# Performance work log

Measured on AMD Instinct MI355X. Metric: run time of the kernel, lower is better.

The kernel has to match this reference:

```python
import jax, jax.numpy as jnp
import numpy as np

B, D, N, H = 2, 512, 2048, 8
DK = D // H
EPS = 1e-5


def conv1x1(x, w, b):
    # kernel-size-1 Conv1d == channel-mixing GEMM: (o,i) x (b,i,n) -> (b,o,n)
    return jnp.einsum('oi,bin->bon', w, x) + b[None, :, None]


def setup_inputs() -> dict:
    key = jax.random.key(0)
    ks = jax.random.split(key, 20)
    s = 0.02
    return {
        'init_query': jax.random.normal(ks[0], (B, D, N), jnp.float32),
        'key_t': jax.random.normal(ks[1], (B, D, N), jnp.float32),
        'value': jax.random.normal(ks[2], (B, D, N), jnp.float32),
        'mask': jax.random.randint(ks[3], (B, 1, N, N), 0, 2, jnp.int32),
        'Wq': jax.random.normal(ks[4], (D, D), jnp.float32) * s,
        'bq': jax.random.normal(ks[5], (D,), jnp.float32) * s,
        'Wk': jax.random.normal(ks[6], (D, D), jnp.float32) * s,
        'bk': jax.random.normal(ks[7], (D,), jnp.float32) * s,
        'Wv': jax.random.normal(ks[8], (D, D), jnp.float32) * s,
        'bv': jax.random.normal(ks[9], (D,), jnp.float32) * s,
        'Wm': jax.random.normal(ks[10], (D, D), jnp.float32) * s,
        'bm': jax.random.normal(ks[11], (D,), jnp.float32) * s,
        'W1': jax.random.normal(ks[12], (2 * D, 2 * D), jnp.float32) * s,
        'b1': jax.random.normal(ks[13], (2 * D,), jnp.float32) * s,
        'gamma': jnp.ones((2 * D,), jnp.float32),
        'beta': jnp.zeros((2 * D,), jnp.float32),
        'rmean': jax.random.normal(ks[14], (2 * D,), jnp.float32) * s,
        'rvar': jnp.abs(jax.random.normal(ks[15], (2 * D,), jnp.float32)) * 0.1 + 0.5,
        'W2': jax.random.normal(ks[16], (D, 2 * D), jnp.float32) * s,
        'b2': jnp.zeros((D,), jnp.float32),  # nn.init.constant_(bias, 0.0)
    }


def reference(init_query, key_t, value, mask, Wq, bq, Wk, bk, Wv, bv, Wm, bm,
              W1, b1, gamma, beta, rmean, rvar, W2, b2):
    # projections, split channels into (d_k, n_heads) exactly like torch .view
    q = conv1x1(init_query, Wq, bq).reshape(B, DK, H, N)
    k = conv1x1(key_t, Wk, bk).reshape(B, DK, H, N)
    v = conv1x1(value, Wv, bv).reshape(B, DK, H, N)
    scores = jnp.einsum('bdhn,bdhm->bhnm', q, k) / jnp.sqrt(jnp.float32(DK))
    scores = jnp.where(mask == 0, jnp.float32(-1e9), scores)
    attn = jax.nn.softmax(scores, axis=-1)
    x = jnp.einsum('bhnm,bdhm->bdhn', attn, v).reshape(B, D, N)
    x = conv1x1(x, Wm, bm)
    x = jnp.concatenate([x, init_query], axis=1)  # (B, 2D, N)
    h = conv1x1(x, W1, b1)
    # BatchNorm1d (inference mode with running stats) + ReLU
    h = (h - rmean[None, :, None]) * (gamma / jnp.sqrt(rvar + EPS))[None, :, None] + beta[None, :, None]
    h = jax.nn.relu(h)
    return conv1x1(h, W2, b2)
```

## Files before the change

### kernel.cpp

```cpp
#include <hip/hip_runtime.h>

typedef unsigned short u16;
typedef unsigned int u32;
typedef unsigned long long u64;
typedef long long i64;
typedef __bf16 bf16x8 __attribute__((ext_vector_type(8)));
typedef u16 u16x8 __attribute__((ext_vector_type(8)));
typedef float f32x4 __attribute__((ext_vector_type(4)));
typedef float f32x16 __attribute__((ext_vector_type(16)));

#define DEV __device__ __forceinline__

constexpr int BB = 2, DD = 512, NN = 2048, HH = 8, DKc = 64, D2 = 1024;

constexpr float QSC = 0.125f * 1.44269504088896340736f;

constexpr i64 MB = 1048576;
constexpr i64 OFF_CAT = 0;
constexpr i64 OFF_XKT = 8 * MB;
constexpr i64 OFF_XVT = 12 * MB;
constexpr i64 OFF_QH  = 16 * MB;
constexpr i64 OFF_KH  = 20 * MB;
constexpr i64 OFF_VT  = 24 * MB;
constexpr i64 OFF_HT  = 28 * MB;
constexpr i64 OFF_OP  = 36 * MB;
constexpr i64 OFF_LP  = 68 * MB;
constexpr i64 OFF_WQP = 69 * MB;
constexpr i64 OFF_WKP = 69 * MB + 524288;
constexpr i64 OFF_WVP = 69 * MB + 1048576;
constexpr i64 OFF_WMT = 69 * MB + 1572864;
constexpr i64 OFF_W1A = 71 * MB;
constexpr i64 OFF_W1C = 72 * MB;
constexpr i64 OFF_W2B = 74 * MB;
constexpr i64 OFF_BQP = 75 * MB;
constexpr i64 OFF_BKP = 75 * MB + 2048;
constexpr i64 OFF_BVP = 75 * MB + 4096;
constexpr i64 OFF_BNA = 75 * MB + 8192;
constexpr i64 OFF_BNC = 75 * MB + 12288;
constexpr i64 OFF_MSK = 76 * MB;

DEV u16 f2bf(float f) {
  u32 u = __float_as_uint(f);
  u = u + 0x7FFFu + ((u >> 16) & 1u);
  return (u16)(u >> 16);
}

DEV float bf2f(u16 u) { return __uint_as_float(((u32)u) << 16); }

DEV u32 packbf(float lo, float hi) {
  return __builtin_amdgcn_perm(__float_as_uint(hi), __float_as_uint(lo), 0x07060302u);
}

DEV float fexp2(float x) {
#if __has_builtin(__builtin_amdgcn_exp2f)
  return __builtin_amdgcn_exp2f(x);
#else
  return exp2f(x);
#endif
}

DEV bf16x8 ldfrag(const u16* p) {
  bf16x8 v;
  __builtin_memcpy(&v, __builtin_assume_aligned(p, 16), 16);
  return v;
}

DEV bf16x8 ldfrag8(const u16* p) {
  bf16x8 v;
  __builtin_memcpy(&v, __builtin_assume_aligned(p, 8), 16);
  return v;
}

DEV bf16x8 ones8() {
  u16x8 u = {0x3F80, 0x3F80, 0x3F80, 0x3F80, 0x3F80, 0x3F80, 0x3F80, 0x3F80};
  bf16x8 v;
  __builtin_memcpy(&v, &u, 16);
  return v;
}

DEV void gload16(const void* g, void* lds) {
  __builtin_amdgcn_global_load_lds((__attribute__((address_space(1))) void*)g,
                                   (__attribute__((address_space(3))) void*)lds, 16, 0, 0);
}

DEV f32x4 mfma16(bf16x8 a, bf16x8 b, f32x4 c) {
  return __builtin_amdgcn_mfma_f32_16x16x32_bf16(a, b, c, 0, 0, 0);
}

DEV f32x16 mfma32(bf16x8 a, bf16x8 b, f32x16 c) {
  return __builtin_amdgcn_mfma_f32_32x32x16_bf16(a, b, c, 0, 0, 0);
}

__global__ __launch_bounds__(256) void prep_all(
    const float* __restrict__ Wq, const float* __restrict__ Wk, const float* __restrict__ Wv,
    const float* __restrict__ Wm, const float* __restrict__ W1, const float* __restrict__ W2,
    const float* __restrict__ bq, const float* __restrict__ bk, const float* __restrict__ bv,
    const float* __restrict__ bm, const float* __restrict__ b1, const float* __restrict__ gamma_,
    const float* __restrict__ beta_, const float* __restrict__ rmean,
    const float* __restrict__ rvar, const int* __restrict__ mask,
    const float* __restrict__ iq, const float* __restrict__ kt, const float* __restrict__ vv,
    u16* __restrict__ wqp, u16* __restrict__ wkp, u16* __restrict__ wvp, u16* __restrict__ wmt,
    u16* __restrict__ w1a, u16* __restrict__ w1c, u16* __restrict__ w2b,
    float* __restrict__ bqp, float* __restrict__ bkp, float* __restrict__ bvp,
    float* __restrict__ bna, float* __restrict__ bnc, u32* __restrict__ mw,
    u16* __restrict__ cat, u16* __restrict__ xkt, u16* __restrict__ xvt) {
  __shared__ float tile[32][33];
  const int blk = blockIdx.x, t = threadIdx.x;
  if (blk < 768) {
    const int which = blk >> 8, lb = blk & 255;
    const float* W = which == 0 ? Wq : (which == 1 ? Wk : Wv);
    u16* dst = which == 0 ? wqp : (which == 1 ? wkp : wvp);
    for (int e = lb * 256 + t; e < 262144; e += 65536) {
      int op = e >> 9, i = e & 511;
      int dk = op & 63, h = op >> 6;
      dst[e] = f2bf(W[(dk * 8 + h) * 512 + i]);
    }
  } else if (blk < 1024) {
    const int lb = blk - 768;
    for (int e = lb * 256 + t; e < 262144; e += 65536) {
      int cp = e >> 9, o = e & 511;
      int dk = cp & 63, h = cp >> 6;
      wmt[e] = f2bf(Wm[o * 512 + dk * 8 + h]);
    }
  } else if (blk < 1280) {
    const int lb = blk - 1024;
    for (int e = lb * 256 + t; e < 524288; e += 65536) {
      int row = e >> 9, o = e & 511;
      w1a[e] = f2bf(W1[(i64)row * 1024 + o]);
    }
  } else if (blk < 1536) {
    const int lb = blk - 1280;
    for (int e = lb * 256 + t; e < 524288; e += 65536) {
      int row = e >> 9, j = e & 511;
      w1c[(i64)row * 1024 + 512 + j] = f2bf(W1[(i64)row * 1024 + 512 + j]);
    }
  } else if (blk < 1792) {
    const int lb = blk - 1536;
    for (int e = lb * 256 + t; e < 524288; e += 65536) w2b[e] = f2bf(W2[e]);
  } else if (blk < 1808) {
    __shared__ float sm[4][64];
    const int base = (blk - 1792) * 64;
    const int el = t & 63, oq = t >> 6;
    const float* wrow = W1 + (i64)(base + el) * 1024 + oq * 128;
    const float* bmq = bm + oq * 128;
    float s = 0.f;
#pragma unroll 8
    for (int j = 0; j < 128; j += 4) {
      float4 x = *(const float4*)(wrow + j);
      float4 y = *(const float4*)(bmq + j);
      s += x.x * y.x + x.y * y.y + x.z * y.z + x.w * y.w;
    }
    sm[oq][el] = s;
    __syncthreads();
    if (t < 64) {
      int e = base + t;
      float a = gamma_[e] * rsqrtf(rvar[e] + 1e-5f);
      bna[e] = a;
      bnc[e] = (b1[e] - rmean[e]) * a + beta_[e] + a * (sm[0][t] + sm[1][t] + sm[2][t] + sm[3][t]);
    }
  } else if (blk == 1808) {
    for (int e = t; e < 512; e += 256) {
      int src = (e & 63) * 8 + (e >> 6);
      bqp[e] = bq[src]; bkp[e] = bk[src]; bvp[e] = bv[src];
    }
  } else if (blk < 2833) {
    const int tid = (blk - 1809) * 256 + t;
    const int l = tid & 63, mt = (tid >> 6) & 31, g = (tid >> 11) & 63, b = tid >> 17;
    const int kv0 = mt * 64 + (l & 31);
    u32 word = 0;
#pragma unroll
    for (int reg = 0; reg < 16; ++reg) {
      int r = (reg & 3) + 8 * (reg >> 2) + 4 * (l >> 5);
      const int* mp = mask + ((i64)b * NN + g * 32 + r) * NN + kv0;
      word |= (mp[0] != 0 ? (1u << (2 * reg)) : 0u) | (mp[32] != 0 ? (2u << (2 * reg)) : 0u);
    }
    mw[tid] = word;
  } else {
    const int idx = blk - 2833;
    const int bx = idx & 63, by = (idx >> 6) & 15, bz = idx >> 10;
    const int tensor = bz >> 1, b = bz & 1;
    const float* src = (tensor == 0 ? iq : (tensor == 1 ? kt : vv)) + (i64)b * DD * NN;
    u16* dst; i64 ldd; int coff;
    if (tensor == 0)      { dst = cat + (i64)b * NN * D2; ldd = D2; coff = DD; }
    else if (tensor == 1) { dst = xkt + (i64)b * NN * DD; ldd = DD; coff = 0; }
    else                  { dst = xvt + (i64)b * NN * DD; ldd = DD; coff = 0; }
    const int x0 = bx * 32, y0 = by * 32;
    const int col = t & 31, rg = t >> 5;
#pragma unroll
    for (int i = 0; i < 4; ++i) {
      int row = rg + i * 8;
      tile[row][col] = src[(i64)(y0 + row) * NN + x0 + col];
    }
    __syncthreads();
    const int dp = t & 15, rbase = t >> 4;
    u32* dst32 = (u32*)dst;
    const i64 ldw = ldd >> 1;
    const int cw = (coff + y0) >> 1;
#pragma unroll
    for (int i = 0; i < 2; ++i) {
      int rr = rbase + i * 16;
      dst32[(i64)(x0 + rr) * ldw + cw + dp] = packbf(tile[2 * dp][rr], tile[2 * dp + 1][rr]);
    }
  }
}

template <int AM, int AN>
DEV void gemm_core(const u16* __restrict__ A, i64 lda, const u16* __restrict__ Bp, i64 ldb,
                   int K, u16* As, u16* Bs, f32x4 (&acc)[AM][AN]) {
  constexpr int BM = AM * 32, BN = AN * 32;
  const int t = threadIdx.x, w = t >> 6, l = t & 63, quad = l >> 4, l15 = l & 15;
  const int wm = (w >> 1) * AM * 16, wn = (w & 1) * AN * 16;
  for (int kk = 0; kk < K; kk += 64) {
    __syncthreads();
#pragma unroll
    for (int j = 0; j < BM / 32; ++j) {
      int ch = j * 256 + w * 64 + l, r = ch >> 3, c = ch & 7;
      gload16(A + (i64)r * lda + kk + ((c ^ (r & 7)) << 3), As + (j * 256 + w * 64) * 8);
    }
#pragma unroll
    for (int j = 0; j < BN / 32; ++j) {
      int ch = j * 256 + w * 64 + l, r = ch >> 3, c = ch & 7;
      gload16(Bp + (i64)r * ldb + kk + ((c ^ (r & 7)) << 3), Bs + (j * 256 + w * 64) * 8);
    }
    __syncthreads();
#pragma unroll
    for (int kc = 0; kc < 2; ++kc) {
      const int sw = ((kc * 4 + quad) ^ (l15 & 7)) << 3;
      bf16x8 af[AM], bfr[AN];
#pragma unroll
      for (int i = 0; i < AM; ++i) af[i] = ldfrag(&As[(wm + i * 16 + l15) * 64 + sw]);
#pragma unroll
      for (int j = 0; j < AN; ++j) bfr[j] = ldfrag(&Bs[(wn + j * 16 + l15) * 64 + sw]);
#pragma unroll
      for (int i = 0; i < AM; ++i)
#pragma unroll
        for (int j = 0; j < AN; ++j) acc[i][j] = mfma16(af[i], bfr[j], acc[i][j]);
    }
  }
}

__global__ __launch_bounds__(256) void qkv_gemm(const u16* __restrict__ cat,
                                                const u16* __restrict__ xkt,
                                                const u16* __restrict__ xvt,
                                                const u16* __restrict__ wqp,
                                                const u16* __restrict__ wkp,
                                                const u16* __restrict__ wvp,
                                                const u16* __restrict__ w1a,
                                                const u16* __restrict__ wmt,
                                                const float* __restrict__ bqp,
                                                const float* __restrict__ bkp,
                                                const float* __restrict__ bvp,
                                                u16* __restrict__ qh, u16* __restrict__ kh,
                                                u16* __restrict__ vt, u16* __restrict__ w1c) {
  __shared__ __align__(16) u16 As[128 * 64];
  __shared__ __align__(16) u16 Bs[64 * 64];
  const int z = blockIdx.z, b = z & 1;
  const int op = (z == 6) ? 3 : (z >> 1);
  const int t = threadIdx.x, w = t >> 6, l = t & 63, quad = l >> 4, l15 = l & 15;
  const int wm = (w >> 1) * 64, wn = (w & 1) * 32;
  int mx, ny;
  const u16 *A, *Bp;
  i64 lda, ldb;
  if (op < 2) {
    mx = blockIdx.x; ny = blockIdx.y;
    A = (op == 0 ? cat + DD : xkt);
    lda = (op == 0 ? D2 : DD);
    A += (i64)b * NN * lda + (i64)mx * 128 * lda;
    Bp = (op == 0 ? wqp : wkp) + (i64)ny * 64 * DD;
    ldb = DD;
  } else if (op == 2) {
    int f = blockIdx.x * 8 + blockIdx.y;
    mx = f >> 5; ny = f & 31;
    A = wvp + (i64)mx * 128 * DD; lda = DD;
    Bp = xvt + (i64)b * NN * DD + (i64)ny * 64 * DD; ldb = DD;
  } else {
    if (blockIdx.x >= 8) return;
    mx = blockIdx.x; ny = blockIdx.y;
    A = w1a + (i64)mx * 128 * DD; lda = DD;
    Bp = wmt + (i64)ny * 64 * DD; ldb = DD;
  }
  f32x4 acc[4][2] = {};
  gemm_core<4, 2>(A, lda, Bp, ldb, DD, As, Bs, acc);

  const int rowBase = mx * 128 + wm + quad * 4;
  const int colBase = ny * 64 + wn + l15;
  if (op < 2) {
    const float* bias = (op == 0 ? bqp : bkp);
    const float sc = (op == 0 ? QSC : 1.f);
    u16* dst = (op == 0 ? qh : kh) + (i64)b * HH * NN * DKc;
#pragma unroll
    for (int j = 0; j < 2; ++j) {
      const int col = colBase + j * 16;
      const float cA = bias[col];
#pragma unroll
      for (int i = 0; i < 4; ++i)
#pragma unroll
        for (int r = 0; r < 4; ++r) {
          const int row = rowBase + i * 16 + r;
          dst[(i64)(col >> 6) * (NN * 64) + (i64)row * 64 + (col & 63)] =
              f2bf((acc[i][j][r] + cA) * sc);
        }
    }
  } else if (op == 2) {
    u16* dst = vt + (i64)b * HH * DKc * NN;
#pragma unroll
    for (int j = 0; j < 2; ++j) {
      const int col = colBase + j * 16;
      const int colp = (col & ~63) | (((col & 31) << 1) | ((col >> 5) & 1));
#pragma unroll
      for (int i = 0; i < 4; ++i)
#pragma unroll
        for (int r = 0; r < 4; ++r) {
          const int row = rowBase + i * 16 + r;
          dst[(i64)row * NN + colp] = f2bf(acc[i][j][r] + bvp[row]);
        }
    }
  } else {
#pragma unroll
    for (int j = 0; j < 2; ++j) {
      const int col = colBase + j * 16;
#pragma unroll
      for (int i = 0; i < 4; ++i)
#pragma unroll
        for (int r = 0; r < 4; ++r) {
          const int row = rowBase + i * 16 + r;
          w1c[(i64)row * D2 + col] = f2bf(acc[i][j][r]);
        }
    }
  }
}

struct GArgs {
  const u16* A; i64 lda, sAb;
  const u16* B; i64 ldb, sBb;
  void* C; i64 ldc, sCb;
  const float* p1; const float* p2;
  int K;
};

template <int MODE, int AM, int AN, int SWZ>
__global__ __launch_bounds__(256) void gemm_bt(GArgs g) {
  __shared__ __align__(16) u16 As[AM * 32 * 64];
  __shared__ __align__(16) u16 Bs[AN * 32 * 64];
  const int t = threadIdx.x, w = t >> 6, l = t & 63, quad = l >> 4, l15 = l & 15;
  const int wm = (w >> 1) * AM * 16, wn = (w & 1) * AN * 16;
  int bx = blockIdx.x, by = blockIdx.y, bz = blockIdx.z;
  if (SWZ == 1) {
    const int i = bx + (by << 3) + (bz << 8);
    const int slot = i & 7, jj = i >> 3;
    by = slot + ((jj & 3) << 3);
    const int j2 = jj >> 2;
    bx = j2 & 7;
    bz = j2 >> 3;
  }
  const u16* A = g.A + (i64)bz * g.sAb + (i64)bx * (AM * 32) * g.lda;
  const u16* Bp = g.B + (i64)bz * g.sBb + (i64)by * (AN * 32) * g.ldb;
  f32x4 acc[AM][AN] = {};
  gemm_core<AM, AN>(A, g.lda, Bp, g.ldb, g.K, As, Bs, acc);

  const int rowBase = bx * (AM * 32) + wm + quad * 4;
  const int colBase = by * (AN * 32) + wn + l15;
#pragma unroll
  for (int j = 0; j < AN; ++j) {
    const int col = colBase + j * 16;
    float cA = 0.f, cB = 0.f;
    if (MODE == 3) { cA = g.p1[col]; cB = g.p2[col]; }
#pragma unroll
    for (int i = 0; i < AM; ++i) {
#pragma unroll
      for (int r = 0; r < 4; ++r) {
        const int row = rowBase + i * 16 + r;
        float v = acc[i][j][r];
        if (MODE == 3) {
          float x = v * cA + cB;
          ((u16*)g.C + (i64)bz * g.sCb)[(i64)row * g.ldc + col] = f2bf(x > 0.f ? x : 0.f);
        } else {
          ((float*)g.C + (i64)bz * g.sCb)[(i64)row * g.ldc + col] = v + g.p1[row];
        }
      }
    }
  }
}

__global__ __launch_bounds__(256) void flash_attn(const u16* __restrict__ Qh,
                                                  const u16* __restrict__ Kh,
                                                  const u16* __restrict__ Vt,
                                                  const u32* __restrict__ MW2,
                                                  u16* __restrict__ Opart,
                                                  float* __restrict__ Lp) {
  __shared__ __align__(16) u16 Ks[64 * 64];
  __shared__ __align__(16) u16 Vs[64 * 64];
  __shared__ __align__(16) u16 Ps[4][32 * 68];
  const int t = threadIdx.x, w = t >> 6, l = t & 63, l31 = l & 31, lh = l >> 5;
  const int flat = blockIdx.x;
  const int h = flat & 7;
  const int j = flat >> 3;
  const int nt = j & 15, zz = j >> 4;
  const int b = zz >> 2, sp = zz & 3;
  const u16* Qb = Qh + ((i64)(b * HH + h) * NN + nt * 128 + w * 32) * 64;
  const u16* Kb = Kh + (i64)(b * HH + h) * NN * 64;
  const u16* Vb = Vt + (i64)(b * HH + h) * 64 * NN;
  const u32* MWb = MW2 + ((i64)(b * 64 + nt * 4 + w) * 32) * 64 + l;
  const bf16x8 ONE = ones8();
  bf16x8 qf[4];
#pragma unroll
  for (int kc = 0; kc < 4; ++kc)
    __builtin_memcpy(&qf[kc], Qb + (i64)l31 * 64 + kc * 16 + lh * 8, 16);

  f32x16 oacc0 = {}, oacc1 = {}, lacc = {};
  for (int mt = sp * 8; mt < sp * 8 + 8; ++mt) {
    __syncthreads();
#pragma unroll
    for (int j2 = 0; j2 < 2; ++j2) {
      int ch = j2 * 256 + t, r = ch >> 3, c = ch & 7;
      gload16(Kb + (i64)(mt * 64 + r) * 64 + ((c ^ (r & 7)) << 3), &Ks[ch * 8]);
      gload16(Vb + (i64)r * NN + mt * 64 + ((c ^ (r & 7)) << 3), &Vs[ch * 8]);
    }
    __syncthreads();
    f32x16 s0 = {}, s1 = {};
#pragma unroll
    for (int kc = 0; kc < 4; ++kc) {
      const int r1 = 32 + l31;
      bf16x8 k0 = ldfrag(&Ks[l31 * 64 + (((kc * 2 + lh) ^ (l31 & 7)) << 3)]);
      bf16x8 k1 = ldfrag(&Ks[r1 * 64 + (((kc * 2 + lh) ^ (r1 & 7)) << 3)]);
      s0 = mfma32(qf[kc], k0, s0);
      s1 = mfma32(qf[kc], k1, s1);
    }
    const u32 mword = MWb[(i64)mt * 64];
#pragma unroll
    for (int reg = 0; reg < 16; ++reg) {
      const int row = (reg & 3) + 8 * (reg >> 2) + 4 * lh;
      u32 sh = mword >> (2 * reg);
      u32 m01 = ((sh & 1u) | ((sh & 2u) << 15)) * 0xFFFFu;
      u32 pv = packbf(fexp2(s0[reg]), fexp2(s1[reg])) & m01;
      *(u32*)__builtin_assume_aligned(&Ps[w][row * 68 + l31 * 2], 4) = pv;
    }
    asm volatile("" ::: "memory");
    bf16x8 pf[4];
#pragma unroll
    for (int kc = 0; kc < 4; ++kc) pf[kc] = ldfrag8(&Ps[w][l31 * 68 + kc * 16 + lh * 8]);
#pragma unroll
    for (int kc = 0; kc < 4; ++kc) lacc = mfma32(pf[kc], ONE, lacc);
#pragma unroll
    for (int kc = 0; kc < 4; ++kc) {
      const int r1 = 32 + l31;
      bf16x8 v0 = ldfrag(&Vs[l31 * 64 + (((kc * 2 + lh) ^ (l31 & 7)) << 3)]);
      bf16x8 v1 = ldfrag(&Vs[r1 * 64 + (((kc * 2 + lh) ^ (r1 & 7)) << 3)]);
      oacc0 = mfma32(pf[kc], v0, oacc0);
      oacc1 = mfma32(pf[kc], v1, oacc1);
    }
  }
  u16* Op = Opart + (i64)sp * (BB * NN * DD) + ((i64)b * NN + nt * 128 + w * 32) * DD + h * 64;
#pragma unroll
  for (int reg = 0; reg < 16; ++reg) {
    const int row = (reg & 3) + 8 * (reg >> 2) + 4 * lh;
    Op[(i64)row * DD + l31] = f2bf(oacc0[reg]);
    Op[(i64)row * DD + 32 + l31] = f2bf(oacc1[reg]);
  }
  if (l31 == 0) {
    float* Lpb = Lp + ((i64)(sp * BB + b) * HH + h) * NN + nt * 128 + w * 32;
#pragma unroll
    for (int reg = 0; reg < 16; ++reg)
      Lpb[(reg & 3) + 8 * (reg >> 2) + 4 * lh] = lacc[reg];
  }
}

__global__ __launch_bounds__(256) void combine(const u16* __restrict__ Opart,
                                               const float* __restrict__ Lp,
                                               u16* __restrict__ cat) {
  const int tid = blockIdx.x * 256 + threadIdx.x;
  const int b = tid >> 17, rem = tid & 131071;
  const int n = rem >> 6, cg = rem & 63;
  const int c0 = cg << 3, h = cg >> 3;
  const i64 base = ((i64)b * NN + n) * DD + c0;
  const i64 stride = (i64)BB * NN * DD;
  float acc[8] = {};
  float lsum = 0.f;
#pragma unroll
  for (int s = 0; s < 4; ++s) {
    u16 a[8];
    __builtin_memcpy(a, __builtin_assume_aligned(Opart + s * stride + base, 16), 16);
#pragma unroll
    for (int j = 0; j < 8; ++j) acc[j] += bf2f(a[j]);
    lsum += Lp[((i64)(s * BB + b) * HH + h) * NN + n];
  }
  float rl = __builtin_amdgcn_rcpf(lsum);
  u16 o[8];
#pragma unroll
  for (int j = 0; j < 8; ++j) o[j] = f2bf(acc[j] * rl);
  __builtin_memcpy(__builtin_assume_aligned(&cat[((i64)b * NN + n) * D2 + c0], 16), o, 16);
}

extern "C" void kernel_launch(void* const* d_in, const int* in_sizes, int n_in,
                              void* d_out, int out_size, void* d_ws, size_t ws_size,
                              hipStream_t stream) {
  (void)in_sizes; (void)n_in; (void)out_size; (void)ws_size;
  const float* iq    = (const float*)d_in[0];
  const float* kt    = (const float*)d_in[1];
  const float* vv    = (const float*)d_in[2];
  const int*   mask  = (const int*)d_in[3];
  const float* Wq    = (const float*)d_in[4];
  const float* bq    = (const float*)d_in[5];
  const float* Wk    = (const float*)d_in[6];
  const float* bk    = (const float*)d_in[7];
  const float* Wv    = (const float*)d_in[8];
  const float* bv    = (const float*)d_in[9];
  const float* Wm    = (const float*)d_in[10];
  const float* bm    = (const float*)d_in[11];
  const float* W1    = (const float*)d_in[12];
  const float* b1    = (const float*)d_in[13];
  const float* gamma_= (const float*)d_in[14];
  const float* beta_ = (const float*)d_in[15];
  const float* rmean = (const float*)d_in[16];
  const float* rvar  = (const float*)d_in[17];
  const float* W2    = (const float*)d_in[18];
  const float* b2    = (const float*)d_in[19];

  char* ws = (char*)d_ws;
  u16* cat = (u16*)(ws + OFF_CAT);
  u16* xkt = (u16*)(ws + OFF_XKT);
  u16* xvt = (u16*)(ws + OFF_XVT);
  u16* qh  = (u16*)(ws + OFF_QH);
  u16* kh  = (u16*)(ws + OFF_KH);
  u16* vt  = (u16*)(ws + OFF_VT);
  u16* ht  = (u16*)(ws + OFF_HT);
  u16* opart = (u16*)(ws + OFF_OP);
  float* lp  = (float*)(ws + OFF_LP);
  u16* wqp = (u16*)(ws + OFF_WQP);
  u16* wkp = (u16*)(ws + OFF_WKP);
  u16* wvp = (u16*)(ws + OFF_WVP);
  u16* wmt = (u16*)(ws + OFF_WMT);
  u16* w1a = (u16*)(ws + OFF_W1A);
  u16* w1c = (u16*)(ws + OFF_W1C);
  u16* w2b = (u16*)(ws + OFF_W2B);
  float* bqp = (float*)(ws + OFF_BQP);
  float* bkp = (float*)(ws + OFF_BKP);
  float* bvp = (float*)(ws + OFF_BVP);
  float* bna = (float*)(ws + OFF_BNA);
  float* bnc = (float*)(ws + OFF_BNC);
  u32* mw = (u32*)(ws + OFF_MSK);

  prep_all<<<8977, 256, 0, stream>>>(Wq, Wk, Wv, Wm, W1, W2, bq, bk, bv, bm, b1, gamma_, beta_,
                                     rmean, rvar, mask, iq, kt, vv, wqp, wkp, wvp, wmt, w1a, w1c,
                                     w2b, bqp, bkp, bvp, bna, bnc, mw, cat, xkt, xvt);
  qkv_gemm<<<dim3(16, 8, 7), 256, 0, stream>>>(cat, xkt, xvt, wqp, wkp, wvp, w1a, wmt,
                                               bqp, bkp, bvp, qh, kh, vt, w1c);
  flash_attn<<<1024, 256, 0, stream>>>(qh, kh, vt, mw, opart, lp);
  combine<<<1024, 256, 0, stream>>>(opart, lp, cat);
  GArgs wa{cat, D2, 0, w1c, D2, 0, ht, D2, 0, bna, bnc, D2};
  gemm_bt<3, 4, 2, 0><<<dim3(32, 16, 1), 256, 0, stream>>>(wa);
  GArgs w2a{w2b, D2, 0, ht, D2, (i64)NN * D2, d_out, NN, (i64)DD * NN, b2, nullptr, D2};
  gemm_bt<4, 2, 2, 1><<<dim3(8, 32, 2), 256, 0, stream>>>(w2a);
}
```

Before: 222.3 us.

## Compute transposed S in flash attention to keep P in registers, drop LDS staging

The attention kernel now computes S^T by swapping the MFMA operands, so the exponentiated probabilities land directly in register fragments usable as the B operand of the PV and row-sum MFMAs. This removes the per-wave LDS round trip for P. The mask is repacked as a contiguous row-major bitmask built with int4 loads, and the V layout permutation is dropped in favour of split 8-byte fragment loads. Opart is written transposed (d-major), so the combine kernel becomes an LDS-transposing tile kernel. The risk is strided scalar stores of Opart and extra LDS traffic in combine.

```diff
diff --git a/kernel.cpp b/kernel.cpp
--- a/kernel.cpp
+++ b/kernel.cpp
@@ -46,6 +46,7 @@
 }
 
 DEV float bf2f(u16 u) { return __uint_as_float(((u32)u) << 16); }
+DEV float bf2f32(u32 u) { return __uint_as_float(u << 16); }
 
 DEV u32 packbf(float lo, float hi) {
   return __builtin_amdgcn_perm(__float_as_uint(hi), __float_as_uint(lo), 0x07060302u);
@@ -65,9 +66,10 @@
   return v;
 }
 
-DEV bf16x8 ldfrag8(const u16* p) {
+DEV bf16x8 ldfrag2(const u16* p0, const u16* p1) {
   bf16x8 v;
-  __builtin_memcpy(&v, __builtin_assume_aligned(p, 8), 16);
+  __builtin_memcpy(&v, __builtin_assume_aligned(p0, 8), 8);
+  __builtin_memcpy((char*)&v + 8, __builtin_assume_aligned(p1, 8), 8);
   return v;
 }
 
@@ -165,14 +167,15 @@
     }
   } else if (blk < 2833) {
     const int tid = (blk - 1809) * 256 + t;
-    const int l = tid & 63, mt = (tid >> 6) & 31, g = (tid >> 11) & 63, b = tid >> 17;
-    const int kv0 = mt * 64 + (l & 31);
+    const i64 base = (i64)tid * 32;
+    const int4* mp = (const int4*)(mask + base);
     u32 word = 0;
 #pragma unroll
-    for (int reg = 0; reg < 16; ++reg) {
-      int r = (reg & 3) + 8 * (reg >> 2) + 4 * (l >> 5);
-      const int* mp = mask + ((i64)b * NN + g * 32 + r) * NN + kv0;
-      word |= (mp[0] != 0 ? (1u << (2 * reg)) : 0u) | (mp[32] != 0 ? (2u << (2 * reg)) : 0u);
+    for (int j = 0; j < 8; ++j) {
+      int4 x = mp[j];
+      u32 nib = (x.x != 0 ? 1u : 0u) | (x.y != 0 ? 2u : 0u) | (x.z != 0 ? 4u : 0u) |
+                (x.w != 0 ? 8u : 0u);
+      word |= nib << (j * 4);
     }
     mw[tid] = word;
   } else {
@@ -306,13 +309,12 @@
 #pragma unroll
     for (int j = 0; j < 2; ++j) {
       const int col = colBase + j * 16;
-      const int colp = (col & ~63) | (((col & 31) << 1) | ((col >> 5) & 1));
 #pragma unroll
       for (int i = 0; i < 4; ++i)
 #pragma unroll
         for (int r = 0; r < 4; ++r) {
           const int row = rowBase + i * 16 + r;
-          dst[(i64)row * NN + colp] = f2bf(acc[i][j][r] + bvp[row]);
+          dst[(i64)row * NN + col] = f2bf(acc[i][j][r] + bvp[row]);
         }
     }
   } else {
@@ -385,22 +387,22 @@
 __global__ __launch_bounds__(256) void flash_attn(const u16* __restrict__ Qh,
                                                   const u16* __restrict__ Kh,
                                                   const u16* __restrict__ Vt,
-                                                  const u32* __restrict__ MW2,
+                                                  const u64* __restrict__ MW64,
                                                   u16* __restrict__ Opart,
                                                   float* __restrict__ Lp) {
   __shared__ __align__(16) u16 Ks[64 * 64];
   __shared__ __align__(16) u16 Vs[64 * 64];
-  __shared__ __align__(16) u16 Ps[4][32 * 68];
   const int t = threadIdx.x, w = t >> 6, l = t & 63, l31 = l & 31, lh = l >> 5;
   const int flat = blockIdx.x;
   const int h = flat & 7;
   const int j = flat >> 3;
   const int nt = j & 15, zz = j >> 4;
   const int b = zz >> 2, sp = zz & 3;
+  const int n = nt * 128 + w * 32 + l31;
   const u16* Qb = Qh + ((i64)(b * HH + h) * NN + nt * 128 + w * 32) * 64;
   const u16* Kb = Kh + (i64)(b * HH + h) * NN * 64;
   const u16* Vb = Vt + (i64)(b * HH + h) * 64 * NN;
-  const u32* MWb = MW2 + ((i64)(b * 64 + nt * 4 + w) * 32) * 64 + l;
+  const u64* mwp = MW64 + (i64)(b * NN + n) * 32;
   const bf16x8 ONE = ones8();
   bf16x8 qf[4];
 #pragma unroll
@@ -420,75 +422,90 @@
     f32x16 s0 = {}, s1 = {};
 #pragma unroll
     for (int kc = 0; kc < 4; ++kc) {
-      const int r1 = 32 + l31;
-      bf16x8 k0 = ldfrag(&Ks[l31 * 64 + (((kc * 2 + lh) ^ (l31 & 7)) << 3)]);
-      bf16x8 k1 = ldfrag(&Ks[r1 * 64 + (((kc * 2 + lh) ^ (r1 & 7)) << 3)]);
-      s0 = mfma32(qf[kc], k0, s0);
-      s1 = mfma32(qf[kc], k1, s1);
-    }
-    const u32 mword = MWb[(i64)mt * 64];
-#pragma unroll
-    for (int reg = 0; reg < 16; ++reg) {
-      const int row = (reg & 3) + 8 * (reg >> 2) + 4 * lh;
-      u32 sh = mword >> (2 * reg);
-      u32 m01 = ((sh & 1u) | ((sh & 2u) << 15)) * 0xFFFFu;
-      u32 pv = packbf(fexp2(s0[reg]), fexp2(s1[reg])) & m01;
-      *(u32*)__builtin_assume_aligned(&Ps[w][row * 68 + l31 * 2], 4) = pv;
-    }
-    asm volatile("" ::: "memory");
+      const int sw = l31 & 7;
+      bf16x8 k0 = ldfrag(&Ks[l31 * 64 + (((kc * 2 + lh) ^ sw) << 3)]);
+      bf16x8 k1 = ldfrag(&Ks[(32 + l31) * 64 + (((kc * 2 + lh) ^ sw) << 3)]);
+      s0 = mfma32(k0, qf[kc], s0);
+      s1 = mfma32(k1, qf[kc], s1);
+    }
+    const u64 mrow = mwp[mt];
+    u32 pw[16];
+#pragma unroll
+    for (int k = 0; k < 8; ++k) {
+      const int kvb = ((2 * k) & 3) + 8 * ((2 * k) >> 2) + 4 * lh;
+      u64 sh = mrow >> kvb;
+      u32 mA = (((u32)sh & 1u) | (((u32)sh & 2u) << 15)) * 0xFFFFu;
+      u32 shh = (u32)(sh >> 32);
+      u32 mB = ((shh & 1u) | ((shh & 2u) << 15)) * 0xFFFFu;
+      pw[k] = packbf(fexp2(s0[2 * k]), fexp2(s0[2 * k + 1])) & mA;
+      pw[8 + k] = packbf(fexp2(s1[2 * k]), fexp2(s1[2 * k + 1])) & mB;
+    }
     bf16x8 pf[4];
 #pragma unroll
-    for (int kc = 0; kc < 4; ++kc) pf[kc] = ldfrag8(&Ps[w][l31 * 68 + kc * 16 + lh * 8]);
-#pragma unroll
-    for (int kc = 0; kc < 4; ++kc) lacc = mfma32(pf[kc], ONE, lacc);
-#pragma unroll
-    for (int kc = 0; kc < 4; ++kc) {
-      const int r1 = 32 + l31;
-      bf16x8 v0 = ldfrag(&Vs[l31 * 64 + (((kc * 2 + lh) ^ (l31 & 7)) << 3)]);
-      bf16x8 v1 = ldfrag(&Vs[r1 * 64 + (((kc * 2 + lh) ^ (r1 & 7)) << 3)]);
-      oacc0 = mfma32(pf[kc], v0, oacc0);
-      oacc1 = mfma32(pf[kc], v1, oacc1);
-    }
-  }
-  u16* Op = Opart + (i64)sp * (BB * NN * DD) + ((i64)b * NN + nt * 128 + w * 32) * DD + h * 64;
-#pragma unroll
-  for (int reg = 0; reg < 16; ++reg) {
-    const int row = (reg & 3) + 8 * (reg >> 2) + 4 * lh;
-    Op[(i64)row * DD + l31] = f2bf(oacc0[reg]);
-    Op[(i64)row * DD + 32 + l31] = f2bf(oacc1[reg]);
-  }
-  if (l31 == 0) {
-    float* Lpb = Lp + ((i64)(sp * BB + b) * HH + h) * NN + nt * 128 + w * 32;
-#pragma unroll
-    for (int reg = 0; reg < 16; ++reg)
-      Lpb[(reg & 3) + 8 * (reg >> 2) + 4 * lh] = lacc[reg];
-  }
+    for (int c = 0; c < 4; ++c) __builtin_memcpy(&pf[c], &pw[c * 4], 16);
+#pragma unroll
+    for (int c = 0; c < 4; ++c) lacc = mfma32(ONE, pf[c], lacc);
+#pragma unroll
+    for (int c = 0; c < 4; ++c) {
+      const int sw0 = l31 & 7;
+      const u16* r0 = &Vs[l31 * 64];
+      const u16* r1 = &Vs[(32 + l31) * 64];
+      bf16x8 v0 = ldfrag2(r0 + (((2 * c) ^ sw0) << 3) + lh * 4,
+                          r0 + (((2 * c + 1) ^ sw0) << 3) + lh * 4);
+      bf16x8 v1 = ldfrag2(r1 + (((2 * c) ^ sw0) << 3) + lh * 4,
+                          r1 + (((2 * c + 1) ^ sw0) << 3) + lh * 4);
+      oacc0 = mfma32(v0, pf[c], oacc0);
+      oacc1 = mfma32(v1, pf[c], oacc1);
+    }
+  }
+  u16* OpT = Opart + ((i64)((sp * BB + b) * HH + h) * 64) * NN;
+#pragma unroll
+  for (int r = 0; r < 16; ++r) {
+    const int d0 = (r & 3) + 8 * (r >> 2) + 4 * lh;
+    OpT[(i64)d0 * NN + n] = f2bf(oacc0[r]);
+    OpT[(i64)(d0 + 32) * NN + n] = f2bf(oacc1[r]);
+  }
+  if (lh == 0) Lp[((i64)(sp * BB + b) * HH + h) * NN + n] = lacc[0];
 }
 
 __global__ __launch_bounds__(256) void combine(const u16* __restrict__ Opart,
                                                const float* __restrict__ Lp,
                                                u16* __restrict__ cat) {
-  const int tid = blockIdx.x * 256 + threadIdx.x;
-  const int b = tid >> 17, rem = tid & 131071;
-  const int n = rem >> 6, cg = rem & 63;
-  const int c0 = cg << 3, h = cg >> 3;
-  const i64 base = ((i64)b * NN + n) * DD + c0;
-  const i64 stride = (i64)BB * NN * DD;
-  float acc[8] = {};
-  float lsum = 0.f;
-#pragma unroll
-  for (int s = 0; s < 4; ++s) {
-    u16 a[8];
-    __builtin_memcpy(a, __builtin_assume_aligned(Opart + s * stride + base, 16), 16);
-#pragma unroll
-    for (int j = 0; j < 8; ++j) acc[j] += bf2f(a[j]);
-    lsum += Lp[((i64)(s * BB + b) * HH + h) * NN + n];
-  }
-  float rl = __builtin_amdgcn_rcpf(lsum);
-  u16 o[8];
-#pragma unroll
-  for (int j = 0; j < 8; ++j) o[j] = f2bf(acc[j] * rl);
-  __builtin_memcpy(__builtin_assume_aligned(&cat[((i64)b * NN + n) * D2 + c0], 16), o, 16);
+  __shared__ float lt[128 * 65];
+  const int t = threadIdx.x;
+  const int nt = blockIdx.x, bh = blockIdx.y;
+  const int b = bh >> 3, h = bh & 7;
+  const int n0 = nt * 128;
+  const i64 sstride = (i64)BB * HH * 64 * NN;
+  const u16* Ob = Opart + ((i64)(b * HH + h) * 64) * NN;
+#pragma unroll
+  for (int i = 0; i < 16; ++i) {
+    const int idx = i * 256 + t;
+    const int d = idx >> 6, np = idx & 63;
+    float sa = 0.f, sb = 0.f;
+#pragma unroll
+    for (int s = 0; s < 4; ++s) {
+      u32 v;
+      __builtin_memcpy(&v, Ob + s * sstride + (i64)d * NN + n0 + 2 * np, 4);
+      sa += bf2f32(v & 0xFFFFu);
+      sb += bf2f32(v >> 16);
+    }
+    lt[(2 * np) * 65 + d] = sa;
+    lt[(2 * np + 1) * 65 + d] = sb;
+  }
+  __syncthreads();
+  u32* catw = (u32*)cat;
+#pragma unroll
+  for (int i = 0; i < 16; ++i) {
+    const int idx = i * 256 + t;
+    const int nn = idx >> 5, dp = idx & 31;
+    float lsum = 0.f;
+#pragma unroll
+    for (int s = 0; s < 4; ++s) lsum += Lp[((i64)(s * BB + b) * HH + h) * NN + n0 + nn];
+    const float rl = __builtin_amdgcn_rcpf(lsum);
+    u32 pv = packbf(lt[nn * 65 + 2 * dp] * rl, lt[nn * 65 + 2 * dp + 1] * rl);
+    catw[((i64)b * NN + n0 + nn) * (D2 / 2) + h * 32 + dp] = pv;
+  }
 }
 
 extern "C" void kernel_launch(void* const* d_in, const int* in_sizes, int n_in,
@@ -545,8 +562,8 @@
                                      w2b, bqp, bkp, bvp, bna, bnc, mw, cat, xkt, xvt);
   qkv_gemm<<<dim3(16, 8, 7), 256, 0, stream>>>(cat, xkt, xvt, wqp, wkp, wvp, w1a, wmt,
                                                bqp, bkp, bvp, qh, kh, vt, w1c);
-  flash_attn<<<1024, 256, 0, stream>>>(qh, kh, vt, mw, opart, lp);
-  combine<<<1024, 256, 0, stream>>>(opart, lp, cat);
+  flash_attn<<<1024, 256, 0, stream>>>(qh, kh, vt, (const u64*)mw, opart, lp);
+  combine<<<dim3(16, 16), 256, 0, stream>>>(opart, lp, cat);
   GArgs wa{cat, D2, 0, w1c, D2, 0, ht, D2, 0, bna, bnc, D2};
   gemm_bt<3, 4, 2, 0><<<dim3(32, 16, 1), 256, 0, stream>>>(wa);
   GArgs w2a{w2b, D2, 0, ht, D2, (i64)NN * D2, d_out, NN, (i64)DD * NN, b2, nullptr, D2};
```

Result: no change. 220.9 us (-0.6%).
